# Kernel tuning notes

Hardware: AMD Instinct MI355X
Metric: run time of the kernel (lower is better)

The kernel has to match this reference:

```python
import jax, jax.numpy as jnp
import numpy as np

B, T, I, H = 512, 1024, 50, 32  # batch, seq_len, input_size, hidden_size


def setup_inputs() -> dict:
    key = jax.random.key(0)
    ks = jax.random.split(key, 13)
    s = 1.0 / np.sqrt(H)  # PyTorch LSTM/Linear uniform init bound

    def u(k, shape):
        return jax.random.uniform(k, shape, jnp.float32, -s, s)

    return {
        "x": jax.random.normal(ks[0], (B, T, I), jnp.float32),
        # forward direction LSTM params (gate order: i, f, g, o)
        "w_ih_f": u(ks[1], (4 * H, I)),
        "w_hh_f": u(ks[2], (4 * H, H)),
        "b_ih_f": u(ks[3], (4 * H,)),
        "b_hh_f": u(ks[4], (4 * H,)),
        # reverse direction LSTM params
        "w_ih_r": u(ks[5], (4 * H, I)),
        "w_hh_r": u(ks[6], (4 * H, H)),
        "b_ih_r": u(ks[7], (4 * H,)),
        "b_hh_r": u(ks[8], (4 * H,)),
        # FC head
        "fc1_w": u(ks[9], (2 * H, 2 * H)),
        "fc1_b": u(ks[10], (2 * H,)),
        "fc3_w": u(ks[11], (1, 2 * H)),
        "fc3_b": u(ks[12], (1,)),
    }


def _lstm_scan(x_proj, w_hh):
    # x_proj: (T, B, 4H) = precomputed input projections + biases
    b = x_proj.shape[1]
    h0 = jnp.zeros((b, H), x_proj.dtype)
    c0 = jnp.zeros((b, H), x_proj.dtype)

    def step(carry, xp):
        h, c = carry
        z = xp + h @ w_hh.T  # (B, 4H)
        i, f, g, o = jnp.split(z, 4, axis=-1)
        c = jax.nn.sigmoid(f) * c + jax.nn.sigmoid(i) * jnp.tanh(g)
        h = jax.nn.sigmoid(o) * jnp.tanh(c)
        return (h, c), h

    _, hs = jax.lax.scan(step, (h0, c0), x_proj)
    return hs  # (T, B, H)


def reference(x, w_ih_f, w_hh_f, b_ih_f, b_hh_f,
              w_ih_r, w_hh_r, b_ih_r, b_hh_r,
              fc1_w, fc1_b, fc3_w, fc3_b):
    xt = jnp.swapaxes(x, 0, 1)  # (T, B, I) time-major for scan
    # batch all input projections up front (big GEMM instead of per-step)
    pf = xt @ w_ih_f.T + (b_ih_f + b_hh_f)          # (T, B, 4H)
    pr = xt[::-1] @ w_ih_r.T + (b_ih_r + b_hh_r)    # reversed time

    hf = _lstm_scan(pf, w_hh_f)           # (T, B, H)
    hr = _lstm_scan(pr, w_hh_r)[::-1]     # flip back to forward time order

    out = jnp.concatenate([hf, hr], axis=-1)  # (T, B, 2H)
    out = jnp.swapaxes(out, 0, 1)             # (B, T, 2H)
    out = out @ fc1_w.T + fc1_b               # fc1
    # dropout(p=0.2) is identity in eval/inference mode
    out = out @ fc3_w.T + fc3_b               # fc3 -> (B, T, 1)
    return out
```

## Files before the change

kernel.cpp:

```cpp
#include <hip/hip_runtime.h>

#define BB 512
#define TT 1024
#define II 50
#define HH 32
#define CH 16
#define NCH (TT / CH)
#define RSLOT 32

typedef float v2f __attribute__((ext_vector_type(2)));
typedef float v4f __attribute__((ext_vector_type(4)));
typedef short v8s __attribute__((ext_vector_type(8)));

__device__ __forceinline__ float fast_rcp(float x) { return __builtin_amdgcn_rcpf(x); }
__device__ __forceinline__ float sigm(float x) { return fast_rcp(1.f + __expf(-x)); }
__device__ __forceinline__ float tanh_(float x) {
    return 1.f - 2.f * fast_rcp(1.f + __expf(2.f * x));
}
__device__ __forceinline__ float hadd(v2f v) { return v.x + v.y; }
__device__ __forceinline__ short bf16rne(float f) {
    unsigned u = __float_as_uint(f);
    u += 0x7FFF + ((u >> 16) & 1);
    return (short)(u >> 16);
}

__global__ void init_out_kernel(float* __restrict__ out,
                                const float* __restrict__ fc1_b,
                                const float* __restrict__ fc3_w,
                                const float* __restrict__ fc3_b,
                                int n) {
    int idx = blockIdx.x * blockDim.x + threadIdx.x;
    float b = fc3_b[0];
    #pragma unroll
    for (int k = 0; k < 64; ++k) b += fc3_w[k] * fc1_b[k];
    if (idx < n) out[idx] = b;
}

__global__ void __launch_bounds__(128, 1) lstm_pc_kernel(
    const float* __restrict__ x,
    const float* __restrict__ w_ih_f, const float* __restrict__ w_hh_f,
    const float* __restrict__ b_ih_f, const float* __restrict__ b_hh_f,
    const float* __restrict__ w_ih_r, const float* __restrict__ w_hh_r,
    const float* __restrict__ b_ih_r, const float* __restrict__ b_hh_r,
    const float* __restrict__ fc1_w, const float* __restrict__ fc3_w,
    float* __restrict__ out)
{
    __shared__ float ringF[RSLOT * 256];
    __shared__ float hbuf[2][HH][65];
    __shared__ __align__(16) float hst[64];

    const int tid  = threadIdx.x;
    const int lane = tid & 63;
    const int wave = tid >> 6;
    const int b    = blockIdx.x;
    float* outb = out + (size_t)b * TT;

    if (wave == 1) {
        const float* xb = x + (size_t)b * TT * II;
        const int nl = lane & 15;
        const int q  = lane >> 4;
        const float* wih[2] = {w_ih_f, w_ih_r};

        v8s Bf[2][8][2];
        #pragma unroll
        for (int d = 0; d < 2; ++d)
            #pragma unroll
            for (int nt = 0; nt < 8; ++nt) {
                const int n = nt * 16 + nl;
                #pragma unroll
                for (int kf = 0; kf < 2; ++kf)
                    #pragma unroll
                    for (int j = 0; j < 8; ++j) {
                        const int k = kf * 32 + q * 8 + j;
                        Bf[d][nt][kf][j] = (k < II) ? bf16rne(wih[d][n * II + k])
                                                    : (short)0;
                    }
            }

        auto cidx = [](int g) -> int {
            return (g < 32) ? 2 * g
                 : (g < 64) ? 2 * (g - 32) + 1
                 : (g < 96) ? 64 + 2 * (g - 64)
                            : 64 + 2 * (g - 96) + 1;
        };

        auto produce_chunk = [&](int c) {
            #pragma unroll
            for (int d = 0; d < 2; ++d) {
                const int S = c * CH + nl;
                const int t = d ? (TT - 1 - S) : S;
                const float* xr = xb + (size_t)t * II;
                v8s A0, A1;
                #pragma unroll
                for (int j = 0; j < 8; ++j) A0[j] = bf16rne(xr[q * 8 + j]);
                #pragma unroll
                for (int j = 0; j < 8; ++j) {
                    const int k = 32 + q * 8 + j;
                    A1[j] = (k < II) ? bf16rne(xr[k]) : (short)0;
                }
                #pragma unroll
                for (int nt = 0; nt < 8; ++nt) {
                    v4f acc = {0.f, 0.f, 0.f, 0.f};
                    acc = __builtin_amdgcn_mfma_f32_16x16x32_bf16(A0, Bf[d][nt][0], acc, 0, 0, 0);
                    acc = __builtin_amdgcn_mfma_f32_16x16x32_bf16(A1, Bf[d][nt][1], acc, 0, 0, 0);
                    const int col = d * 128 + cidx(nt * 16 + nl);
                    #pragma unroll
                    for (int r = 0; r < 4; ++r) {
                        const int slot = (c * CH + q * 4 + r) & (RSLOT - 1);
                        ringF[slot * 256 + col] = acc[r];
                    }
                }
            }
        };
        auto flush = [&](int m) {
            if (lane < 32) {
                const int d   = lane >> 4;
                const int idx = lane & 15;
                const int ti  = m * CH + idx;
                const int col = ti & 63;
                float d0 = 0.f, d1 = 0.f, d2 = 0.f, d3 = 0.f;
                #pragma unroll
                for (int k = 0; k < HH; k += 4) {
                    d0 += hbuf[d][k    ][col];
                    d1 += hbuf[d][k + 1][col];
                    d2 += hbuf[d][k + 2][col];
                    d3 += hbuf[d][k + 3][col];
                }
                const int t = d ? (TT - 1 - ti) : ti;
                atomicAdd(&outb[t], (d0 + d1) + (d2 + d3));
            }
        };

        produce_chunk(0);
        __syncthreads();
        for (int n = 0; n < NCH; ++n) {
            if (n + 1 < NCH) produce_chunk(n + 1);
            if (n >= 1) flush(n - 1);
            __syncthreads();
        }
        flush(NCH - 1);
    } else {
        const int d = lane >> 5;
        const int k = lane & 31;
        const float* w_hh = d ? w_hh_r : w_hh_f;
        const float* bi   = d ? b_ih_r : b_ih_f;
        const float* bh   = d ? b_hh_r : b_hh_f;

        v2f wp[4][16];
        float bb[4];
        #pragma unroll
        for (int D = 0; D < 4; ++D) {
            const int row = D * 32 + k;
            #pragma unroll
            for (int j = 0; j < 16; ++j) {
                wp[D][j].x = w_hh[row * HH + 2 * j];
                wp[D][j].y = w_hh[row * HH + 2 * j + 1];
            }
            bb[D] = bi[row] + bh[row];
        }

        float wc = 0.f;
        {
            const int j = d * HH + k;
            #pragma unroll
            for (int n = 0; n < 64; ++n) wc += fc3_w[n] * fc1_w[n * 64 + j];
        }

        hst[lane] = 0.f;
        float c = 0.f;

        __syncthreads();

        for (int n = 0; n < NCH; ++n) {
            const int slot0 = (n & 1) * CH;
            const int col0  = (n & 3) * CH;
            #pragma unroll
            for (int u = 0; u < CH; ++u) {
                const float* rp = &ringF[(slot0 + u) * 256 + d * 128 + 2 * k];
                const v2f xz1 = *(const v2f*)rp;
                const v2f xz2 = *(const v2f*)(rp + 64);

                float4 h4[8];
                #pragma unroll
                for (int j = 0; j < 8; ++j)
                    h4[j] = *(const float4*)&hst[d * 32 + 4 * j];

                v2f aA[4], aB[4];
                #pragma unroll
                for (int D = 0; D < 4; ++D) {
                    aA[D] = (v2f){bb[D], 0.f};
                    aB[D] = (v2f){0.f, 0.f};
                }
                #pragma unroll
                for (int j = 0; j < 8; ++j) {
                    v2f p0 = {h4[j].x, h4[j].y};
                    v2f p1 = {h4[j].z, h4[j].w};
                    #pragma unroll
                    for (int D = 0; D < 4; ++D) {
                        aA[D] = __builtin_elementwise_fma(p0, wp[D][2 * j    ], aA[D]);
                        aB[D] = __builtin_elementwise_fma(p1, wp[D][2 * j + 1], aB[D]);
                    }
                }
                const float zi = xz1.x + hadd(aA[0] + aB[0]);
                const float zf = xz1.y + hadd(aA[1] + aB[1]);
                const float zg = xz2.x + hadd(aA[2] + aB[2]);
                const float zo = xz2.y + hadd(aA[3] + aB[3]);

                const float gi = sigm(zi);
                const float gf = sigm(zf);
                const float gg = tanh_(zg);
                const float go = sigm(zo);

                c = fmaf(gf, c, gi * gg);
                const float h = go * tanh_(c);

                hst[lane] = h;
                hbuf[d][k][col0 + u] = h * wc;
                asm volatile("" ::: "memory");
            }
            __syncthreads();
        }
    }
}

extern "C" void kernel_launch(void* const* d_in, const int* in_sizes, int n_in,
                              void* d_out, int out_size, void* d_ws, size_t ws_size,
                              hipStream_t stream) {
    const float* x      = (const float*)d_in[0];
    const float* w_ih_f = (const float*)d_in[1];
    const float* w_hh_f = (const float*)d_in[2];
    const float* b_ih_f = (const float*)d_in[3];
    const float* b_hh_f = (const float*)d_in[4];
    const float* w_ih_r = (const float*)d_in[5];
    const float* w_hh_r = (const float*)d_in[6];
    const float* b_ih_r = (const float*)d_in[7];
    const float* b_hh_r = (const float*)d_in[8];
    const float* fc1_w  = (const float*)d_in[9];
    const float* fc1_b  = (const float*)d_in[10];
    const float* fc3_w  = (const float*)d_in[11];
    const float* fc3_b  = (const float*)d_in[12];
    float* out = (float*)d_out;

    const int n = BB * TT;
    init_out_kernel<<<(n + 255) / 256, 256, 0, stream>>>(out, fc1_b, fc3_w, fc3_b, n);

    lstm_pc_kernel<<<BB, 128, 0, stream>>>(
        x, w_ih_f, w_hh_f, b_ih_f, b_hh_f,
        w_ih_r, w_hh_r, b_ih_r, b_hh_r,
        fc1_w, fc3_w, out);
}
```

Before: 430.5 us.

## Split LSTM recurrence across two waves with half-K lanes and permlane reduction

The recurrent step moves from one wave handling both directions to one wave per direction, with 192 threads per block. Within each wave, the two 32-lane halves each take half of the hidden-size dot product and combine the partial sums through a permlane32 swap (or a shuffle fallback). This halves the per-lane FMA issue work and register weight footprint on the serial critical path. In exchange it adds a cross-lane exchange per gate per step, a third wave per block, and duplicated gate and state math across lane halves.

```diff
diff --git a/kernel.cpp b/kernel.cpp
--- a/kernel.cpp
+++ b/kernel.cpp
@@ -17,12 +17,24 @@
 __device__ __forceinline__ float tanh_(float x) {
     return 1.f - 2.f * fast_rcp(1.f + __expf(2.f * x));
 }
-__device__ __forceinline__ float hadd(v2f v) { return v.x + v.y; }
 __device__ __forceinline__ short bf16rne(float f) {
     unsigned u = __float_as_uint(f);
     u += 0x7FFF + ((u >> 16) & 1);
     return (short)(u >> 16);
 }
+
+#if __has_builtin(__builtin_amdgcn_permlane32_swap)
+typedef unsigned v2u __attribute__((ext_vector_type(2)));
+__device__ __forceinline__ float xhalf_sum(float p) {
+    v2u r = __builtin_amdgcn_permlane32_swap(__float_as_uint(p),
+                                             __float_as_uint(p), false, false);
+    return __uint_as_float(r.x) + __uint_as_float(r.y);
+}
+#else
+__device__ __forceinline__ float xhalf_sum(float p) {
+    return p + __shfl_xor(p, 32, 64);
+}
+#endif
 
 __global__ void init_out_kernel(float* __restrict__ out,
                                 const float* __restrict__ fc1_b,
@@ -36,7 +48,7 @@
     if (idx < n) out[idx] = b;
 }
 
-__global__ void __launch_bounds__(128, 1) lstm_pc_kernel(
+__global__ void __launch_bounds__(192, 1) lstm_pc_kernel(
     const float* __restrict__ x,
     const float* __restrict__ w_ih_f, const float* __restrict__ w_hh_f,
     const float* __restrict__ b_ih_f, const float* __restrict__ b_hh_f,
@@ -55,7 +67,7 @@
     const int b    = blockIdx.x;
     float* outb = out + (size_t)b * TT;
 
-    if (wave == 1) {
+    if (wave == 2) {
         const float* xb = x + (size_t)b * TT * II;
         const int nl = lane & 15;
         const int q  = lane >> 4;
@@ -140,23 +152,24 @@
         }
         flush(NCH - 1);
     } else {
-        const int d = lane >> 5;
-        const int k = lane & 31;
+        const int d  = wave;
+        const int k  = lane & 31;
+        const int kh = lane >> 5;
         const float* w_hh = d ? w_hh_r : w_hh_f;
         const float* bi   = d ? b_ih_r : b_ih_f;
         const float* bh   = d ? b_hh_r : b_hh_f;
 
-        v2f wp[4][16];
-        float bb[4];
+        v2f wp[4][8];
+        float bseed[4];
         #pragma unroll
         for (int D = 0; D < 4; ++D) {
             const int row = D * 32 + k;
             #pragma unroll
-            for (int j = 0; j < 16; ++j) {
-                wp[D][j].x = w_hh[row * HH + 2 * j];
-                wp[D][j].y = w_hh[row * HH + 2 * j + 1];
-            }
-            bb[D] = bi[row] + bh[row];
+            for (int j = 0; j < 8; ++j) {
+                wp[D][j].x = w_hh[row * HH + 16 * kh + 2 * j];
+                wp[D][j].y = w_hh[row * HH + 16 * kh + 2 * j + 1];
+            }
+            bseed[D] = kh ? 0.f : (bi[row] + bh[row]);
         }
 
         float wc = 0.f;
@@ -166,7 +179,7 @@
             for (int n = 0; n < 64; ++n) wc += fc3_w[n] * fc1_w[n * 64 + j];
         }
 
-        hst[lane] = 0.f;
+        hst[d * 32 + k] = 0.f;
         float c = 0.f;
 
         __syncthreads();
@@ -180,31 +193,28 @@
                 const v2f xz1 = *(const v2f*)rp;
                 const v2f xz2 = *(const v2f*)(rp + 64);
 
-                float4 h4[8];
-                #pragma unroll
-                for (int j = 0; j < 8; ++j)
-                    h4[j] = *(const float4*)&hst[d * 32 + 4 * j];
-
-                v2f aA[4], aB[4];
-                #pragma unroll
-                for (int D = 0; D < 4; ++D) {
-                    aA[D] = (v2f){bb[D], 0.f};
-                    aB[D] = (v2f){0.f, 0.f};
-                }
-                #pragma unroll
-                for (int j = 0; j < 8; ++j) {
+                float4 h4[4];
+                #pragma unroll
+                for (int j = 0; j < 4; ++j)
+                    h4[j] = *(const float4*)&hst[d * 32 + kh * 16 + 4 * j];
+
+                v2f acc[4];
+                #pragma unroll
+                for (int D = 0; D < 4; ++D) acc[D] = (v2f){bseed[D], 0.f};
+                #pragma unroll
+                for (int j = 0; j < 4; ++j) {
                     v2f p0 = {h4[j].x, h4[j].y};
                     v2f p1 = {h4[j].z, h4[j].w};
                     #pragma unroll
                     for (int D = 0; D < 4; ++D) {
-                        aA[D] = __builtin_elementwise_fma(p0, wp[D][2 * j    ], aA[D]);
-                        aB[D] = __builtin_elementwise_fma(p1, wp[D][2 * j + 1], aB[D]);
+                        acc[D] = __builtin_elementwise_fma(p0, wp[D][2 * j    ], acc[D]);
+                        acc[D] = __builtin_elementwise_fma(p1, wp[D][2 * j + 1], acc[D]);
                     }
                 }
-                const float zi = xz1.x + hadd(aA[0] + aB[0]);
-                const float zf = xz1.y + hadd(aA[1] + aB[1]);
-                const float zg = xz2.x + hadd(aA[2] + aB[2]);
-                const float zo = xz2.y + hadd(aA[3] + aB[3]);
+                const float zi = xhalf_sum(acc[0].x + acc[0].y) + xz1.x;
+                const float zf = xhalf_sum(acc[1].x + acc[1].y) + xz1.y;
+                const float zg = xhalf_sum(acc[2].x + acc[2].y) + xz2.x;
+                const float zo = xhalf_sum(acc[3].x + acc[3].y) + xz2.y;
 
                 const float gi = sigm(zi);
                 const float gf = sigm(zf);
@@ -214,7 +224,7 @@
                 c = fmaf(gf, c, gi * gg);
                 const float h = go * tanh_(c);
 
-                hst[lane] = h;
+                hst[d * 32 + k] = h;
                 hbuf[d][k][col0 + u] = h * wc;
                 asm volatile("" ::: "memory");
             }
@@ -244,7 +254,7 @@
     const int n = BB * TT;
     init_out_kernel<<<(n + 255) / 256, 256, 0, stream>>>(out, fc1_b, fc3_w, fc3_b, n);
 
-    lstm_pc_kernel<<<BB, 128, 0, stream>>>(
+    lstm_pc_kernel<<<BB, 192, 0, stream>>>(
         x, w_ih_f, w_hh_f, b_ih_f, b_hh_f,
         w_ih_r, w_hh_r, b_ih_r, b_hh_r,
         fc1_w, fc3_w, out);
```

New measurement: 632.3 us. +46.9%, slower.
